# Kernel optimization log

Hardware: AMD Instinct MI355X
Metric: run time of the kernel (lower is better)

## Reference

```python
import jax, jax.numpy as jnp
import numpy as np

B, H, SQ, SKV, D = 4, 16, 2048, 2048, 128
SCALE = float(np.sqrt(D))  # scale_factor passed to forward; q_k is divided by it


def setup_inputs() -> dict:
    key = jax.random.key(0)
    kq, kk, kv = jax.random.split(key, 3)
    q = jax.random.normal(kq, (B, H, SQ, D), dtype=jnp.float32)
    k = jax.random.normal(kk, (B, H, SKV, D), dtype=jnp.float32)
    v = jax.random.normal(kv, (B, H, SKV, D), dtype=jnp.float32)
    return {"q": q, "k": k, "v": v}


def reference(q, k, v):
    # q_k = q @ k^T, divided by scale_factor
    scores = jnp.einsum("bhqd,bhkd->bhqk", q, k) / SCALE  # [B,H,Sq,Skv]
    attn = jax.nn.softmax(scores, axis=-1)
    # dropout(p=0.1) is identity in eval/inference mode
    out = jnp.einsum("bhqk,bhkd->bhqd", attn, v)  # [B,H,Sq,D]
    return out
```

## Files before the change

### kernel.cpp

```cpp
#include <hip/hip_runtime.h>
#include <hip/hip_bf16.h>

#define B_ 4
#define H_ 16
#define SQ 2048
#define SKV 2048
#define D_ 128
#define BH (B_*H_)
#define BM 128
#define BN 64
#define NITER (SKV/BN)

typedef __attribute__((ext_vector_type(8))) short bf16x8;
typedef __attribute__((ext_vector_type(4))) float f32x4;

__device__ inline unsigned short f2bf(float f) {
    union { float f; unsigned u; } x{f};
    unsigned r = x.u + 0x7fffu + ((x.u >> 16) & 1u);
    return (unsigned short)(r >> 16);
}

#if defined(__has_builtin) && __has_builtin(__builtin_amdgcn_cvt_pk_bf16_f32)
#define PKBF16(a,b) ({ auto _r = __builtin_amdgcn_cvt_pk_bf16_f32((a),(b)); \
                       unsigned _u; __builtin_memcpy(&_u, &_r, 4); _u; })
#else
#define PKBF16(a,b) ((unsigned)f2bf(a) | ((unsigned)f2bf(b) << 16))
#endif

__device__ inline void gl_lds16(const short* g, short* l) {
    __builtin_amdgcn_global_load_lds((const __attribute__((address_space(1))) unsigned*)g,
                                     (__attribute__((address_space(3))) unsigned*)l,
                                     16, 0, 0);
}

__global__ __launch_bounds__(256) void prep(const float* __restrict__ kin,
                                            const float* __restrict__ vin,
                                            short* __restrict__ kbf,
                                            short* __restrict__ vtg) {
    __shared__ short tile[64 * 136];
    int bx = blockIdx.x, tid = threadIdx.x;
    if (bx < 8192) {
        const float4* s = (const float4*)kin;
        uint2* d = (uint2*)kbf;
        int i = bx * 256 + tid;
        const int HALF = (BH * SKV * D_ / 4) / 2;
#pragma unroll
        for (int h = 0; h < 2; ++h) {
            int j = i + h * HALF;
            float4 a = s[j];
            d[j] = make_uint2(PKBF16(a.x, a.y), PKBF16(a.z, a.w));
        }
    } else {
        int bx2 = bx - 8192;
        int bh = bx2 >> 5;
        int t0 = (bx2 & 31) * 64;
        {
            int r = tid >> 4, cg = tid & 15;
#pragma unroll
            for (int s = 0; s < 4; ++s) {
                int rr = r + s * 16;
                const float* p = vin + ((size_t)bh * SKV + t0 + rr) * D_ + cg * 8;
                float4 a = *(const float4*)p;
                float4 b = *(const float4*)(p + 4);
                union { unsigned u[4]; bf16x8 v; } f;
                f.u[0] = PKBF16(a.x, a.y); f.u[1] = PKBF16(a.z, a.w);
                f.u[2] = PKBF16(b.x, b.y); f.u[3] = PKBF16(b.z, b.w);
                *(bf16x8*)&tile[rr * 136 + cg * 8] = f.v;
            }
        }
        __syncthreads();
        {
            int d = tid >> 1, h2 = tid & 1;
#pragma unroll
            for (int s = 0; s < 4; ++s) {
                int kv = h2 * 32 + s * 8;
                union { short u[8]; uint4 q; } o;
#pragma unroll
                for (int j = 0; j < 8; ++j) o.u[j] = tile[(kv + j) * 136 + d];
                *(uint4*)(vtg + ((size_t)bh * D_ + d) * SKV + t0 + kv) = o.q;
            }
        }
    }
}

__global__ __launch_bounds__(256, 3) void fa_kernel(const float* __restrict__ q,
                                                    const short* __restrict__ kbf,
                                                    const short* __restrict__ vtg,
                                                    float* __restrict__ out) {
    __shared__ short Ksh[64 * 128];
    __shared__ short Vsh[128 * 64];
    __shared__ short Psh[4 * 32 * 72];

    const int tid = threadIdx.x;
    const int wave = tid >> 6;
    const int lane = tid & 63;
    const int l16 = lane & 15;
    const int quad = lane >> 4;

    const int bx = blockIdx.x;
    const int qt = bx & 15;
    const int bh = bx >> 4;
    const int qrow0 = qt * BM + wave * 32;

    const float cscale = 1.4426950408889634f * 0.08838834764831845f;

    bf16x8 qf[2][4];
#pragma unroll
    for (int mt = 0; mt < 2; ++mt) {
        int row = qrow0 + mt * 16 + l16;
        const float* qp = q + ((size_t)bh * SQ + row) * D_ + quad * 8;
#pragma unroll
        for (int ks = 0; ks < 4; ++ks) {
            const float* p = qp + ks * 32;
            float4 a = *(const float4*)p;
            float4 b = *(const float4*)(p + 4);
            union { unsigned u[4]; bf16x8 v; } f;
            f.u[0] = PKBF16(a.x * cscale, a.y * cscale);
            f.u[1] = PKBF16(a.z * cscale, a.w * cscale);
            f.u[2] = PKBF16(b.x * cscale, b.y * cscale);
            f.u[3] = PKBF16(b.z * cscale, b.w * cscale);
            qf[mt][ks] = f.v;
        }
    }

    f32x4 oacc[8][2];
#pragma unroll
    for (int dt = 0; dt < 8; ++dt)
#pragma unroll
        for (int mt = 0; mt < 2; ++mt) oacc[dt][mt] = (f32x4)0.f;
    float lsum[2] = {0.f, 0.f};

    const short* kbase = kbf + (size_t)bh * SKV * D_;
    const short* vbase = vtg + (size_t)bh * D_ * SKV;
    const int krow0 = wave * 4 + (lane >> 4);
    const int kc8 = (lane & 15) ^ krow0;
    const short* kg = kbase + krow0 * 128 + kc8 * 8;
    short* kl = Ksh + wave * 512;
    const int vd0 = wave * 8 + (lane >> 3);
    const int vc = (lane & 7) ^ (lane >> 3);
    const short* vg = vbase + (size_t)vd0 * SKV + vc * 8;
    short* vl = Vsh + wave * 512;

    short* const pwav = Psh + wave * 2304;

    for (int it = 0; it < NITER; ++it) {
        __syncthreads();
#pragma unroll
        for (int s = 0; s < 4; ++s) {
            gl_lds16(kg + s * 2048, kl + s * 2048);
            gl_lds16(vg + (size_t)s * 32 * SKV, vl + s * 2048);
        }
        kg += BN * D_;
        vg += BN;
        __syncthreads();

        f32x4 sacc[4][2];
#pragma unroll
        for (int kt = 0; kt < 4; ++kt) {
            sacc[kt][0] = (f32x4)0.f; sacc[kt][1] = (f32x4)0.f;
        }
#pragma unroll
        for (int kt = 0; kt < 4; ++kt)
#pragma unroll
            for (int ks = 0; ks < 4; ++ks) {
                bf16x8 kf = *(const bf16x8*)&Ksh[(kt * 16 + l16) * 128 + (((ks * 4 + quad) ^ l16) << 3)];
                sacc[kt][0] = __builtin_amdgcn_mfma_f32_16x16x32_bf16(kf, qf[0][ks], sacc[kt][0], 0, 0, 0);
                sacc[kt][1] = __builtin_amdgcn_mfma_f32_16x16x32_bf16(kf, qf[1][ks], sacc[kt][1], 0, 0, 0);
            }

#pragma unroll
        for (int mt = 0; mt < 2; ++mt) {
            short* pw = pwav + (mt * 16 + l16) * 72;
#pragma unroll
            for (int kt = 0; kt < 4; ++kt) {
                float p0 = __builtin_amdgcn_exp2f(sacc[kt][mt][0]);
                float p1 = __builtin_amdgcn_exp2f(sacc[kt][mt][1]);
                float p2 = __builtin_amdgcn_exp2f(sacc[kt][mt][2]);
                float p3 = __builtin_amdgcn_exp2f(sacc[kt][mt][3]);
                lsum[mt] += (p0 + p1) + (p2 + p3);
                *(uint2*)(pw + kt * 16 + quad * 4) = make_uint2(PKBF16(p0, p1), PKBF16(p2, p3));
            }
        }

#pragma unroll
        for (int ks = 0; ks < 2; ++ks) {
            bf16x8 pa0 = *(const bf16x8*)(pwav + l16 * 72 + ks * 32 + quad * 8);
            bf16x8 pa1 = *(const bf16x8*)(pwav + (16 + l16) * 72 + ks * 32 + quad * 8);
#pragma unroll
            for (int dt = 0; dt < 8; ++dt) {
                bf16x8 vf = *(const bf16x8*)&Vsh[(dt * 16 + l16) * 64 + ((((ks * 4 + quad) ^ (l16 & 7))) << 3)];
                oacc[dt][0] = __builtin_amdgcn_mfma_f32_16x16x32_bf16(vf, pa0, oacc[dt][0], 0, 0, 0);
                oacc[dt][1] = __builtin_amdgcn_mfma_f32_16x16x32_bf16(vf, pa1, oacc[dt][1], 0, 0, 0);
            }
        }
    }

#pragma unroll
    for (int mt = 0; mt < 2; ++mt) {
        lsum[mt] += __shfl_xor(lsum[mt], 16);
        lsum[mt] += __shfl_xor(lsum[mt], 32);
    }
    const float rl[2] = {1.0f / lsum[0], 1.0f / lsum[1]};
#pragma unroll
    for (int mt = 0; mt < 2; ++mt) {
        float* op = out + ((size_t)bh * SQ + qrow0 + mt * 16 + l16) * D_ + quad * 4;
#pragma unroll
        for (int dt = 0; dt < 8; ++dt) {
            f32x4 v = oacc[dt][mt] * rl[mt];
            *(f32x4*)(op + dt * 16) = v;
        }
    }
}

extern "C" void kernel_launch(void* const* d_in, const int* in_sizes, int n_in,
                              void* d_out, int out_size, void* d_ws, size_t ws_size,
                              hipStream_t stream) {
    const float* q = (const float*)d_in[0];
    const float* k = (const float*)d_in[1];
    const float* v = (const float*)d_in[2];
    float* out = (float*)d_out;

    short* kbf = (short*)d_ws;
    short* vtg = kbf + (size_t)BH * SKV * D_;

    prep<<<8192 + 2048, 256, 0, stream>>>(k, v, kbf, vtg);
    fa_kernel<<<BH * (SQ / BM), 256, 0, stream>>>(q, kbf, vtg, out);
}
```

Measured before the change: 373.2 us.

## Switch attention to 32x32x16 MFMA and keep P in registers via permlane32 swap

The attention kernel moves from 16x16x32 to 32x32x16 bf16 MFMA tiles. The softmax probabilities are reshuffled across lane halves with permlane32_swap so they feed the PV matmul straight from registers, which drops the per-wave LDS staging buffer and its stores and loads. The V prep kernel also transposes through register pairs instead of an LDS tile with a barrier. The costs are new lane mappings that must match the MFMA layouts and possibly higher register pressure under the 3-block occupancy bound.

```diff
diff --git a/kernel.cpp b/kernel.cpp
--- a/kernel.cpp
+++ b/kernel.cpp
@@ -13,6 +13,7 @@
 
 typedef __attribute__((ext_vector_type(8))) short bf16x8;
 typedef __attribute__((ext_vector_type(4))) float f32x4;
+typedef __attribute__((ext_vector_type(16))) float f32x16;
 
 __device__ inline unsigned short f2bf(float f) {
     union { float f; unsigned u; } x{f};
@@ -33,11 +34,25 @@
                                      16, 0, 0);
 }
 
+__device__ inline void pl32swap(unsigned &a, unsigned &b) {
+#if defined(__has_builtin) && __has_builtin(__builtin_amdgcn_permlane32_swap)
+    auto r = __builtin_amdgcn_permlane32_swap((int)a, (int)b, false, false);
+    unsigned t[2]; __builtin_memcpy(t, &r, 8);
+    a = t[0]; b = t[1];
+#else
+    int lane = threadIdx.x & 63;
+    unsigned ap = __shfl(a, lane ^ 32);
+    unsigned bp = __shfl(b, lane ^ 32);
+    unsigned X = (lane < 32) ? a : bp;
+    unsigned Y = (lane < 32) ? ap : b;
+    a = X; b = Y;
+#endif
+}
+
 __global__ __launch_bounds__(256) void prep(const float* __restrict__ kin,
                                             const float* __restrict__ vin,
                                             short* __restrict__ kbf,
                                             short* __restrict__ vtg) {
-    __shared__ short tile[64 * 136];
     int bx = blockIdx.x, tid = threadIdx.x;
     if (bx < 8192) {
         const float4* s = (const float4*)kin;
@@ -54,32 +69,22 @@
         int bx2 = bx - 8192;
         int bh = bx2 >> 5;
         int t0 = (bx2 & 31) * 64;
-        {
-            int r = tid >> 4, cg = tid & 15;
-#pragma unroll
-            for (int s = 0; s < 4; ++s) {
-                int rr = r + s * 16;
-                const float* p = vin + ((size_t)bh * SKV + t0 + rr) * D_ + cg * 8;
-                float4 a = *(const float4*)p;
-                float4 b = *(const float4*)(p + 4);
-                union { unsigned u[4]; bf16x8 v; } f;
-                f.u[0] = PKBF16(a.x, a.y); f.u[1] = PKBF16(a.z, a.w);
-                f.u[2] = PKBF16(b.x, b.y); f.u[3] = PKBF16(b.z, b.w);
-                *(bf16x8*)&tile[rr * 136 + cg * 8] = f.v;
-            }
-        }
-        __syncthreads();
-        {
-            int d = tid >> 1, h2 = tid & 1;
-#pragma unroll
-            for (int s = 0; s < 4; ++s) {
-                int kv = h2 * 32 + s * 8;
-                union { short u[8]; uint4 q; } o;
-#pragma unroll
-                for (int j = 0; j < 8; ++j) o.u[j] = tile[(kv + j) * 136 + d];
-                *(uint4*)(vtg + ((size_t)bh * D_ + d) * SKV + t0 + kv) = o.q;
-            }
-        }
+        int cp = tid & 63;
+        int g  = tid >> 6;
+        const float* src = vin + ((size_t)bh * SKV + t0 + g * 16) * D_ + cp * 2;
+        unsigned c0[8], c1[8];
+#pragma unroll
+        for (int t = 0; t < 8; ++t) {
+            float2 a = *(const float2*)(src + (size_t)(2 * t) * D_);
+            float2 b = *(const float2*)(src + (size_t)(2 * t + 1) * D_);
+            c0[t] = PKBF16(a.x, b.x);
+            c1[t] = PKBF16(a.y, b.y);
+        }
+        short* dst = vtg + ((size_t)bh * D_ + cp * 2) * SKV + t0 + g * 16;
+        *(uint4*)(dst)            = *(uint4*)&c0[0];
+        *(uint4*)(dst + 8)        = *(uint4*)&c0[4];
+        *(uint4*)(dst + SKV)      = *(uint4*)&c1[0];
+        *(uint4*)(dst + SKV + 8)  = *(uint4*)&c1[4];
     }
 }
 
@@ -89,13 +94,12 @@
                                                     float* __restrict__ out) {
     __shared__ short Ksh[64 * 128];
     __shared__ short Vsh[128 * 64];
-    __shared__ short Psh[4 * 32 * 72];
 
     const int tid = threadIdx.x;
     const int wave = tid >> 6;
     const int lane = tid & 63;
-    const int l16 = lane & 15;
-    const int quad = lane >> 4;
+    const int l32 = lane & 31;
+    const int hi  = lane >> 5;
 
     const int bx = blockIdx.x;
     const int qt = bx & 15;
@@ -104,31 +108,26 @@
 
     const float cscale = 1.4426950408889634f * 0.08838834764831845f;
 
-    bf16x8 qf[2][4];
-#pragma unroll
-    for (int mt = 0; mt < 2; ++mt) {
-        int row = qrow0 + mt * 16 + l16;
-        const float* qp = q + ((size_t)bh * SQ + row) * D_ + quad * 8;
-#pragma unroll
-        for (int ks = 0; ks < 4; ++ks) {
-            const float* p = qp + ks * 32;
-            float4 a = *(const float4*)p;
-            float4 b = *(const float4*)(p + 4);
+    bf16x8 qf[8];
+    {
+        const float* qp = q + ((size_t)bh * SQ + qrow0 + l32) * D_ + hi * 8;
+#pragma unroll
+        for (int dk = 0; dk < 8; ++dk) {
+            float4 a = *(const float4*)(qp + dk * 16);
+            float4 b = *(const float4*)(qp + dk * 16 + 4);
             union { unsigned u[4]; bf16x8 v; } f;
             f.u[0] = PKBF16(a.x * cscale, a.y * cscale);
             f.u[1] = PKBF16(a.z * cscale, a.w * cscale);
             f.u[2] = PKBF16(b.x * cscale, b.y * cscale);
             f.u[3] = PKBF16(b.z * cscale, b.w * cscale);
-            qf[mt][ks] = f.v;
+            qf[dk] = f.v;
         }
     }
 
-    f32x4 oacc[8][2];
-#pragma unroll
-    for (int dt = 0; dt < 8; ++dt)
-#pragma unroll
-        for (int mt = 0; mt < 2; ++mt) oacc[dt][mt] = (f32x4)0.f;
-    float lsum[2] = {0.f, 0.f};
+    f32x16 oacc[4];
+#pragma unroll
+    for (int dt = 0; dt < 4; ++dt) oacc[dt] = (f32x16)0.f;
+    float lsum = 0.f;
 
     const short* kbase = kbf + (size_t)bh * SKV * D_;
     const short* vbase = vtg + (size_t)bh * D_ * SKV;
@@ -141,8 +140,6 @@
     const short* vg = vbase + (size_t)vd0 * SKV + vc * 8;
     short* vl = Vsh + wave * 512;
 
-    short* const pwav = Psh + wave * 2304;
-
     for (int it = 0; it < NITER; ++it) {
         __syncthreads();
 #pragma unroll
@@ -154,62 +151,58 @@
         vg += BN;
         __syncthreads();
 
-        f32x4 sacc[4][2];
-#pragma unroll
-        for (int kt = 0; kt < 4; ++kt) {
-            sacc[kt][0] = (f32x4)0.f; sacc[kt][1] = (f32x4)0.f;
-        }
-#pragma unroll
-        for (int kt = 0; kt < 4; ++kt)
-#pragma unroll
-            for (int ks = 0; ks < 4; ++ks) {
-                bf16x8 kf = *(const bf16x8*)&Ksh[(kt * 16 + l16) * 128 + (((ks * 4 + quad) ^ l16) << 3)];
-                sacc[kt][0] = __builtin_amdgcn_mfma_f32_16x16x32_bf16(kf, qf[0][ks], sacc[kt][0], 0, 0, 0);
-                sacc[kt][1] = __builtin_amdgcn_mfma_f32_16x16x32_bf16(kf, qf[1][ks], sacc[kt][1], 0, 0, 0);
+#pragma unroll
+        for (int kvt = 0; kvt < 2; ++kvt) {
+            f32x16 sacc = (f32x16)0.f;
+#pragma unroll
+            for (int dk = 0; dk < 8; ++dk) {
+                bf16x8 kf = *(const bf16x8*)&Ksh[(kvt * 32 + l32) * 128 + (((dk * 2 + hi) ^ (lane & 15)) << 3)];
+                sacc = __builtin_amdgcn_mfma_f32_32x32x16_bf16(kf, qf[dk], sacc, 0, 0, 0);
             }
 
-#pragma unroll
-        for (int mt = 0; mt < 2; ++mt) {
-            short* pw = pwav + (mt * 16 + l16) * 72;
-#pragma unroll
-            for (int kt = 0; kt < 4; ++kt) {
-                float p0 = __builtin_amdgcn_exp2f(sacc[kt][mt][0]);
-                float p1 = __builtin_amdgcn_exp2f(sacc[kt][mt][1]);
-                float p2 = __builtin_amdgcn_exp2f(sacc[kt][mt][2]);
-                float p3 = __builtin_amdgcn_exp2f(sacc[kt][mt][3]);
-                lsum[mt] += (p0 + p1) + (p2 + p3);
-                *(uint2*)(pw + kt * 16 + quad * 4) = make_uint2(PKBF16(p0, p1), PKBF16(p2, p3));
+            unsigned u[8];
+            float ls = 0.f;
+#pragma unroll
+            for (int t = 0; t < 8; ++t) {
+                float p0 = __builtin_amdgcn_exp2f(sacc[2 * t]);
+                float p1 = __builtin_amdgcn_exp2f(sacc[2 * t + 1]);
+                ls += p0 + p1;
+                u[t] = PKBF16(p0, p1);
             }
-        }
-
-#pragma unroll
-        for (int ks = 0; ks < 2; ++ks) {
-            bf16x8 pa0 = *(const bf16x8*)(pwav + l16 * 72 + ks * 32 + quad * 8);
-            bf16x8 pa1 = *(const bf16x8*)(pwav + (16 + l16) * 72 + ks * 32 + quad * 8);
-#pragma unroll
-            for (int dt = 0; dt < 8; ++dt) {
-                bf16x8 vf = *(const bf16x8*)&Vsh[(dt * 16 + l16) * 64 + ((((ks * 4 + quad) ^ (l16 & 7))) << 3)];
-                oacc[dt][0] = __builtin_amdgcn_mfma_f32_16x16x32_bf16(vf, pa0, oacc[dt][0], 0, 0, 0);
-                oacc[dt][1] = __builtin_amdgcn_mfma_f32_16x16x32_bf16(vf, pa1, oacc[dt][1], 0, 0, 0);
+            lsum += ls;
+
+            pl32swap(u[0], u[2]);
+            pl32swap(u[1], u[3]);
+            pl32swap(u[4], u[6]);
+            pl32swap(u[5], u[7]);
+            union { unsigned w[4]; bf16x8 v; } pf0, pf1;
+            pf0.w[0] = u[0]; pf0.w[1] = u[1]; pf0.w[2] = u[2]; pf0.w[3] = u[3];
+            pf1.w[0] = u[4]; pf1.w[1] = u[5]; pf1.w[2] = u[6]; pf1.w[3] = u[7];
+
+#pragma unroll
+            for (int dt = 0; dt < 4; ++dt) {
+                bf16x8 vf0 = *(const bf16x8*)&Vsh[(dt * 32 + l32) * 64 + (((kvt * 4 + hi) ^ (lane & 7)) << 3)];
+                oacc[dt] = __builtin_amdgcn_mfma_f32_32x32x16_bf16(vf0, pf0.v, oacc[dt], 0, 0, 0);
+                bf16x8 vf1 = *(const bf16x8*)&Vsh[(dt * 32 + l32) * 64 + (((kvt * 4 + 2 + hi) ^ (lane & 7)) << 3)];
+                oacc[dt] = __builtin_amdgcn_mfma_f32_32x32x16_bf16(vf1, pf1.v, oacc[dt], 0, 0, 0);
             }
         }
     }
 
-#pragma unroll
-    for (int mt = 0; mt < 2; ++mt) {
-        lsum[mt] += __shfl_xor(lsum[mt], 16);
-        lsum[mt] += __shfl_xor(lsum[mt], 32);
-    }
-    const float rl[2] = {1.0f / lsum[0], 1.0f / lsum[1]};
-#pragma unroll
-    for (int mt = 0; mt < 2; ++mt) {
-        float* op = out + ((size_t)bh * SQ + qrow0 + mt * 16 + l16) * D_ + quad * 4;
-#pragma unroll
-        for (int dt = 0; dt < 8; ++dt) {
-            f32x4 v = oacc[dt][mt] * rl[mt];
-            *(f32x4*)(op + dt * 16) = v;
-        }
-    }
+    lsum += __shfl_xor(lsum, 32);
+    const float rl = 1.0f / lsum;
+    float* op = out + ((size_t)bh * SQ + qrow0 + l32) * D_ + hi * 4;
+#pragma unroll
+    for (int dt = 0; dt < 4; ++dt)
+#pragma unroll
+        for (int g = 0; g < 4; ++g) {
+            f32x4 v;
+            v[0] = oacc[dt][4 * g + 0] * rl;
+            v[1] = oacc[dt][4 * g + 1] * rl;
+            v[2] = oacc[dt][4 * g + 2] * rl;
+            v[3] = oacc[dt][4 * g + 3] * rl;
+            *(f32x4*)(op + dt * 32 + g * 8) = v;
+        }
 }
 
 extern "C" void kernel_launch(void* const* d_in, const int* in_sizes, int n_in,
```

New measurement: 380.1 us. Within noise of the previous version (+1.8%).
